# Kernel optimization log

Hardware: AMD Instinct MI355X
Metric: run time of the kernel (lower is better)

Reference implementation:

```python
import jax, jax.numpy as jnp
import numpy as np

B, L, S = 8, 8192, 512
DQ, DC = 256, 768
H, DH = 8, 64
INNER = H * DH


def setup_inputs() -> dict:
    key = jax.random.key(0)
    ks = jax.random.split(key, 8)
    std_q = 1.0 / np.sqrt(DQ)
    std_c = 1.0 / np.sqrt(DC)
    std_o = 1.0 / np.sqrt(INNER)
    return {
        "x": jax.random.normal(ks[0], (B, L, DQ), jnp.float32),
        "context": jax.random.normal(ks[1], (B, S, DC), jnp.float32),
        "seq_lens": jax.random.randint(ks[2], (B,), 1, L + 1, jnp.int32),
        "Wq": jax.random.normal(ks[3], (DQ, INNER), jnp.float32) * std_q,
        "Wk": jax.random.normal(ks[4], (DC, INNER), jnp.float32) * std_c,
        "Wv": jax.random.normal(ks[5], (DC, INNER), jnp.float32) * std_c,
        "Wo": jax.random.normal(ks[6], (INNER, DQ), jnp.float32) * std_o,
        "bo": jnp.zeros((DQ,), jnp.float32),
    }


def reference(x, context, seq_lens, Wq, Wk, Wv, Wo, bo):
    # x: [B, L, DQ] padded jagged voxel features; seq_lens: valid count per batch.
    # Equivalent to the per-batch SDPA loop: each batch's queries attend over
    # that batch's full (unmasked) context of S tokens.
    scale = 1.0 / np.sqrt(DH)
    q = (x @ Wq).reshape(B, L, H, DH).transpose(0, 2, 1, 3)        # [B,H,L,DH]
    k = (context @ Wk).reshape(B, S, H, DH).transpose(0, 2, 1, 3)  # [B,H,S,DH]
    v = (context @ Wv).reshape(B, S, H, DH).transpose(0, 2, 1, 3)  # [B,H,S,DH]
    scores = jnp.einsum("bhld,bhsd->bhls", q, k) * scale           # [B,H,L,S]
    attn = jax.nn.softmax(scores, axis=-1)
    out = jnp.einsum("bhls,bhsd->bhld", attn, v)                   # [B,H,L,DH]
    out = out.transpose(0, 2, 1, 3).reshape(B, L, INNER)
    out = out @ Wo + bo                                            # [B,L,DQ]
    valid = (jnp.arange(L)[None, :] < seq_lens[:, None])[..., None]
    return jnp.where(valid, out, 0.0)
```

## Files before the change

kernel.cpp:

```cpp
#include <hip/hip_runtime.h>
#include <hip/hip_bf16.h>

#define DEV __device__ __forceinline__

typedef float f32x4 __attribute__((ext_vector_type(4)));
typedef unsigned short u16x4 __attribute__((ext_vector_type(4)));
typedef unsigned short u16x8 __attribute__((ext_vector_type(8)));
typedef __bf16 bf16x8 __attribute__((ext_vector_type(8)));

DEV unsigned short f2b(float f) { __bf16 h = (__bf16)f; return __builtin_bit_cast(unsigned short, h); }
DEV bf16x8 asbf8(u16x8 v) { return __builtin_bit_cast(bf16x8, v); }

#define MFMA(a, b, c) __builtin_amdgcn_mfma_f32_16x16x32_bf16((a), (b), (c), 0, 0, 0)

constexpr float QSCALE = 0.18033688011112042f;
constexpr float MFIX = 20.0f;

__global__ __launch_bounds__(256) void convert_weights(
    const float* __restrict__ Wq, const float* __restrict__ Wk,
    const float* __restrict__ Wv, const float* __restrict__ Wo,
    unsigned short* __restrict__ WqT, unsigned short* __restrict__ WkvT,
    unsigned short* __restrict__ WoT)
{
  int i = blockIdx.x * 256 + threadIdx.x;
  if (i < 131072) {
    int n = i >> 8, k = i & 255;
    WqT[i] = f2b(Wq[k * 512 + n] * QSCALE);
  } else if (i < 131072 + 786432) {
    int j = i - 131072;
    int n = j / 768, k = j - n * 768;
    float v = (n < 512) ? Wk[k * 512 + n] : Wv[k * 512 + (n - 512)];
    WkvT[j] = f2b(v);
  } else {
    int j = i - 917504;
    int n = j >> 9, k = j & 511;
    WoT[j] = f2b(Wo[k * 256 + n]);
  }
}

template<int KDIM, int NCOLS, int EPI>
DEV void proj_staged(int bx, int by, unsigned short* __restrict__ Lb,
                     const float* __restrict__ Af,
                     const unsigned short* __restrict__ BT,
                     const int* __restrict__ seq_lens,
                     unsigned short* __restrict__ out0,
                     unsigned short* __restrict__ out1)
{
  constexpr int WC = NCOLS / 4;
  constexpr int NCT = WC / 16;
  constexpr int NCH = KDIM / 256;
  constexpr int RS = 264;
  const int t = threadIdx.x;
  const int wid = t >> 6, lane = t & 63;
  const int q = lane & 15, g = lane >> 4;
  const int row0 = bx * 64;
  const int wcol = by * NCOLS + wid * WC;

  if (EPI == 0) {
    const int sl = seq_lens[row0 >> 13];
    if ((row0 & 8191) >= sl) return;
  }

  const int ar0 = t >> 3, akc = (t & 7) * 4;

  const unsigned short* brow[NCT];
  #pragma unroll
  for (int ct = 0; ct < NCT; ++ct)
    brow[ct] = BT + (size_t)(wcol + ct * 16 + q) * KDIM + g * 8;

  f32x4 acc[4][NCT];
  #pragma unroll
  for (int i = 0; i < 4; ++i)
    #pragma unroll
    for (int j = 0; j < NCT; ++j) acc[i][j] = {0.f, 0.f, 0.f, 0.f};

  #pragma unroll 1
  for (int ch = 0; ch < NCH; ++ch) {
    const int kb = ch * 256;
    if (ch) __syncthreads();

    #pragma unroll
    for (int stp = 0; stp < 8; ++stp) {
      const int col = akc + 32 * stp;
      f32x4 v0 = *(const f32x4*)(Af + (size_t)(row0 + ar0) * KDIM + kb + col);
      f32x4 v1 = *(const f32x4*)(Af + (size_t)(row0 + 32 + ar0) * KDIM + kb + col);
      u16x4 w0, w1;
      w0[0] = f2b(v0[0]); w0[1] = f2b(v0[1]); w0[2] = f2b(v0[2]); w0[3] = f2b(v0[3]);
      w1[0] = f2b(v1[0]); w1[1] = f2b(v1[1]); w1[2] = f2b(v1[2]); w1[3] = f2b(v1[3]);
      *(u16x4*)(Lb + ar0 * RS + col) = w0;
      *(u16x4*)(Lb + (32 + ar0) * RS + col) = w1;
    }
    __syncthreads();

    #pragma unroll
    for (int st = 0; st < 8; ++st) {
      const int k0 = st * 32;
      bf16x8 af[4];
      #pragma unroll
      for (int rt = 0; rt < 4; ++rt)
        af[rt] = asbf8(*(const u16x8*)(Lb + (rt * 16 + q) * RS + k0 + g * 8));
      bf16x8 bf[NCT];
      #pragma unroll
      for (int ct = 0; ct < NCT; ++ct)
        bf[ct] = asbf8(*(const u16x8*)(brow[ct] + kb + k0));
      #pragma unroll
      for (int ct = 0; ct < NCT; ++ct)
        #pragma unroll
        for (int rt = 0; rt < 4; ++rt)
          acc[rt][ct] = MFMA(af[rt], bf[ct], acc[rt][ct]);
    }
  }

  if (EPI == 0) {
    const int bb = row0 >> 13, l0 = row0 & 8191;
    #pragma unroll
    for (int ct = 0; ct < NCT; ++ct) {
      int col = wcol + ct * 16 + q;
      int hh = col >> 6, d = col & 63;
      unsigned short* o = out0 + (((size_t)bb * 8 + hh) * 8192) * 64 + d;
      #pragma unroll
      for (int rt = 0; rt < 4; ++rt)
        #pragma unroll
        for (int r = 0; r < 4; ++r) {
          int ll = l0 + rt * 16 + g * 4 + r;
          o[(size_t)ll * 64] = f2b(acc[rt][ct][r]);
        }
    }
  } else {
    const int bb = row0 >> 9, s0 = row0 & 511;
    #pragma unroll
    for (int ct = 0; ct < NCT; ++ct) {
      int col = wcol + ct * 16 + q;
      if (col < 512) {
        int hh = col >> 6, d = col & 63;
        #pragma unroll
        for (int rt = 0; rt < 4; ++rt)
          #pragma unroll
          for (int r = 0; r < 4; ++r) {
            int s = s0 + rt * 16 + g * 4 + r;
            out0[(((size_t)bb * 8 + hh) * 512 + s) * 64 + d] = f2b(acc[rt][ct][r]);
          }
      } else {
        int c2 = col - 512, hh = c2 >> 6, d = c2 & 63;
        #pragma unroll
        for (int rt = 0; rt < 4; ++rt)
          #pragma unroll
          for (int r = 0; r < 4; ++r) {
            int s = s0 + rt * 16 + g * 4 + r;
            out1[(((size_t)bb * 8 + hh) * 64 + d) * 512 + s] = f2b(acc[rt][ct][r]);
          }
      }
    }
  }
}

__global__ __launch_bounds__(256, 4) void qkv_proj(
    const float* __restrict__ x, const float* __restrict__ ctx,
    const unsigned short* __restrict__ WqT, const unsigned short* __restrict__ WkvT,
    const int* __restrict__ seq_lens,
    unsigned short* __restrict__ Qws, unsigned short* __restrict__ Kws,
    unsigned short* __restrict__ VTws)
{
  __shared__ __align__(16) unsigned short Lb[64 * 264];
  const int bid = blockIdx.x;
  if (bid < 512) {
    proj_staged<768, 128, 1>(bid & 63, bid >> 6, Lb,
                             ctx, WkvT, seq_lens, Kws, VTws);
  } else {
    const int j = bid - 512;
    proj_staged<256, 128, 0>(j >> 2, j & 3, Lb,
                             x, WqT, seq_lens, Qws, nullptr);
  }
}

__global__ __launch_bounds__(256, 4) void o_proj(
    const unsigned short* __restrict__ Ab, const unsigned short* __restrict__ WoT,
    const int* __restrict__ seq_lens, float* __restrict__ outf,
    const float* __restrict__ bo)
{
  constexpr int KDIM = 512, NCOLS = 128;
  constexpr int WC = NCOLS / 4;
  constexpr int NCT = WC / 16;
  constexpr int KSTEPS = KDIM / 32;
  constexpr int ASZ = 64 * 40 * 2;
  const int t = threadIdx.x;
  const int wid = t >> 6, lane = t & 63;
  const int q = lane & 15, g = lane >> 4;
  const int row0 = blockIdx.x * 64;
  const int wcol = blockIdx.y * NCOLS + wid * WC;

  const int sl = seq_lens[row0 >> 13];
  if ((row0 & 8191) >= sl) {
    if (blockIdx.y == 0) {
      f32x4 z = {0.f, 0.f, 0.f, 0.f};
      float* o = outf + (size_t)row0 * 256;
      #pragma unroll
      for (int i = 0; i < 16; ++i)
        *(f32x4*)(o + (size_t)(i * 256 + t) * 4) = z;
    }
    return;
  }

  __shared__ __align__(16) char smem[2 * ASZ];

  const int br0 = t >> 2, bkc = (t & 3) * 8;

  f32x4 acc[4][NCT];
  #pragma unroll
  for (int i = 0; i < 4; ++i)
    #pragma unroll
    for (int j = 0; j < NCT; ++j) acc[i][j] = {0.f, 0.f, 0.f, 0.f};

  u16x8 ab;
  ab = *(const u16x8*)(Ab + (size_t)(row0 + br0) * KDIM + bkc);
  *(u16x8*)((unsigned short*)smem + br0 * 40 + bkc) = ab;
  bf16x8 bcur[NCT];
  #pragma unroll
  for (int ct = 0; ct < NCT; ++ct)
    bcur[ct] = asbf8(*(const u16x8*)(WoT + (size_t)(wcol + ct * 16 + q) * KDIM + g * 8));
  __syncthreads();

  #pragma unroll 2
  for (int st = 0; st < KSTEPS; ++st) {
    const int cur = st & 1;
    const int k1 = (st + 1) * 32;

    if (st + 1 < KSTEPS)
      ab = *(const u16x8*)(Ab + (size_t)(row0 + br0) * KDIM + k1 + bkc);
    bf16x8 bnx[NCT];
    if (st + 1 < KSTEPS) {
      #pragma unroll
      for (int ct = 0; ct < NCT; ++ct)
        bnx[ct] = asbf8(*(const u16x8*)(WoT + (size_t)(wcol + ct * 16 + q) * KDIM + k1 + g * 8));
    }

    bf16x8 af[4];
    {
      const unsigned short* Lb = (const unsigned short*)(smem + cur * ASZ);
      #pragma unroll
      for (int rt = 0; rt < 4; ++rt)
        af[rt] = asbf8(*(const u16x8*)(Lb + (rt * 16 + q) * 40 + g * 8));
    }

    #pragma unroll
    for (int ct = 0; ct < NCT; ++ct)
      #pragma unroll
      for (int rt = 0; rt < 4; ++rt)
        acc[rt][ct] = MFMA(af[rt], bcur[ct], acc[rt][ct]);

    if (st + 1 < KSTEPS) {
      *(u16x8*)((unsigned short*)(smem + (cur ^ 1) * ASZ) + br0 * 40 + bkc) = ab;
      #pragma unroll
      for (int ct = 0; ct < NCT; ++ct) bcur[ct] = bnx[ct];
    }
    __syncthreads();
  }

  const int l0 = row0 & 8191;
  #pragma unroll
  for (int ct = 0; ct < NCT; ++ct) {
    int col = wcol + ct * 16 + q;
    float bias = bo[col];
    #pragma unroll
    for (int rt = 0; rt < 4; ++rt)
      #pragma unroll
      for (int r = 0; r < 4; ++r) {
        int ll = l0 + rt * 16 + g * 4 + r;
        float v = acc[rt][ct][r] + bias;
        outf[(size_t)(row0 + rt * 16 + g * 4 + r) * 256 + col] = (ll < sl) ? v : 0.f;
      }
  }
}

__global__ __launch_bounds__(256, 4) void attn_kernel(
    const unsigned short* __restrict__ Qw, const unsigned short* __restrict__ Kw,
    const unsigned short* __restrict__ VTw, const int* __restrict__ seq_lens,
    unsigned short* __restrict__ AO)
{
  const int bid = blockIdx.x;
  const int h = bid & 7;
  const int tile = (bid >> 3) & 63;
  const int b = bid >> 9;

  const int sl = seq_lens[b];
  const int qbase0 = tile * 128;
  if (qbase0 >= sl) return;

  const int wid = threadIdx.x >> 6, lane = threadIdx.x & 63;
  const int q = lane & 15, g = lane >> 4;

  __shared__ __align__(16) unsigned short Ks[2][32 * 64];
  __shared__ __align__(16) unsigned short Vs[2][64 * 32];

  const int krow  = (wid << 3) + (lane >> 3);
  const int kslot = (lane & 7) ^ (lane >> 3);
  const int vd    = (wid << 4) + (lane >> 2);
  const int vc    = lane & 3;
  const int vswz  = (vd >> 1) & 3;
  const int vs0   = (((2 * vc) & 3) ^ vswz) * 8 + ((vc >> 1) * 4);
  const int vs1   = (((2 * vc + 1) & 3) ^ vswz) * 8 + ((vc >> 1) * 4);
  const int vrslot = (g ^ ((q >> 1) & 3)) * 8;

  const int qbase = qbase0 + wid * 32;
  const bool wactive = qbase < sl;

  const unsigned short* Qb = Qw + (((size_t)b * 8 + h) * 8192 + qbase) * 64;
  const unsigned short* Kb = Kw + ((size_t)b * 8 + h) * (512 * 64);
  const unsigned short* Vb = VTw + ((size_t)b * 8 + h) * (64 * 512);

  bf16x8 qf[2][2];
  if (wactive) {
    #pragma unroll
    for (int qt = 0; qt < 2; ++qt)
      #pragma unroll
      for (int dc = 0; dc < 2; ++dc)
        qf[qt][dc] = asbf8(*(const u16x8*)(Qb + (qt * 16 + q) * 64 + dc * 32 + g * 8));
  }

  f32x4 acc[2][4];
  float lsum[2] = {0.f, 0.f};
  #pragma unroll
  for (int qt = 0; qt < 2; ++qt)
    #pragma unroll
    for (int dt = 0; dt < 4; ++dt) acc[qt][dt] = {0.f, 0.f, 0.f, 0.f};

  {
    u16x8 kr = *(const u16x8*)(Kb + krow * 64 + (lane & 7) * 8);
    u16x8 vr = *(const u16x8*)(Vb + vd * 512 + vc * 8);
    *(u16x8*)(&Ks[0][krow * 64 + kslot * 8]) = kr;
    u16x4 vlo, vhi;
    vlo[0] = vr[0]; vlo[1] = vr[1]; vlo[2] = vr[2]; vlo[3] = vr[3];
    vhi[0] = vr[4]; vhi[1] = vr[5]; vhi[2] = vr[6]; vhi[3] = vr[7];
    *(u16x4*)(&Vs[0][vd * 32 + vs0]) = vlo;
    *(u16x4*)(&Vs[0][vd * 32 + vs1]) = vhi;
  }
  __syncthreads();

  #pragma unroll 2
  for (int st = 0; st < 16; ++st) {
    const int cur = st & 1;
    const int scn = (st + 1) * 32;

    u16x8 kn, vn;
    if (st < 15) {
      kn = *(const u16x8*)(Kb + (scn + krow) * 64 + (lane & 7) * 8);
      vn = *(const u16x8*)(Vb + vd * 512 + scn + vc * 8);
    }

    if (wactive) {
      bf16x8 kf[2][2];
      #pragma unroll
      for (int tt = 0; tt < 2; ++tt)
        #pragma unroll
        for (int dc = 0; dc < 2; ++dc)
          kf[tt][dc] = asbf8(*(const u16x8*)(
              &Ks[cur][(tt * 16 + q) * 64 + ((dc * 4 + g) ^ (q & 7)) * 8]));

      bf16x8 va[4];
      #pragma unroll
      for (int dt = 0; dt < 4; ++dt)
        va[dt] = asbf8(*(const u16x8*)(&Vs[cur][(dt * 16 + q) * 32 + vrslot]));

      #pragma unroll
      for (int qt = 0; qt < 2; ++qt) {
        f32x4 t0 = {-MFIX, -MFIX, -MFIX, -MFIX};
        f32x4 t1 = {-MFIX, -MFIX, -MFIX, -MFIX};
        t0 = MFMA(kf[0][0], qf[qt][0], t0);
        t0 = MFMA(kf[0][1], qf[qt][1], t0);
        t1 = MFMA(kf[1][0], qf[qt][0], t1);
        t1 = MFMA(kf[1][1], qf[qt][1], t1);

        float p0 = __builtin_amdgcn_exp2f(t0[0]);
        float p1 = __builtin_amdgcn_exp2f(t0[1]);
        float p2 = __builtin_amdgcn_exp2f(t0[2]);
        float p3 = __builtin_amdgcn_exp2f(t0[3]);
        float p4 = __builtin_amdgcn_exp2f(t1[0]);
        float p5 = __builtin_amdgcn_exp2f(t1[1]);
        float p6 = __builtin_amdgcn_exp2f(t1[2]);
        float p7 = __builtin_amdgcn_exp2f(t1[3]);
        lsum[qt] += ((p0 + p1) + (p2 + p3)) + ((p4 + p5) + (p6 + p7));

        u16x8 pu;
        pu[0] = f2b(p0); pu[1] = f2b(p1); pu[2] = f2b(p2); pu[3] = f2b(p3);
        pu[4] = f2b(p4); pu[5] = f2b(p5); pu[6] = f2b(p6); pu[7] = f2b(p7);
        bf16x8 pb = asbf8(pu);

        #pragma unroll
        for (int dt = 0; dt < 4; ++dt)
          acc[qt][dt] = MFMA(va[dt], pb, acc[qt][dt]);
      }
    }

    if (st < 15) {
      const int nb = cur ^ 1;
      *(u16x8*)(&Ks[nb][krow * 64 + kslot * 8]) = kn;
      u16x4 vlo, vhi;
      vlo[0] = vn[0]; vlo[1] = vn[1]; vlo[2] = vn[2]; vlo[3] = vn[3];
      vhi[0] = vn[4]; vhi[1] = vn[5]; vhi[2] = vn[6]; vhi[3] = vn[7];
      *(u16x4*)(&Vs[nb][vd * 32 + vs0]) = vlo;
      *(u16x4*)(&Vs[nb][vd * 32 + vs1]) = vhi;
    }
    __syncthreads();
  }

  if (wactive) {
    #pragma unroll
    for (int qt = 0; qt < 2; ++qt) {
      float lt = lsum[qt];
      lt += __shfl_xor(lt, 16);
      lt += __shfl_xor(lt, 32);
      float inv = __builtin_amdgcn_rcpf(lt);
      size_t ro = ((size_t)b * 8192 + qbase + qt * 16 + q) * 512 + h * 64;
      #pragma unroll
      for (int dt = 0; dt < 4; ++dt) {
        u16x4 o;
        o[0] = f2b(acc[qt][dt][0] * inv);
        o[1] = f2b(acc[qt][dt][1] * inv);
        o[2] = f2b(acc[qt][dt][2] * inv);
        o[3] = f2b(acc[qt][dt][3] * inv);
        *(u16x4*)(AO + ro + dt * 16 + g * 4) = o;
      }
    }
  }
}

extern "C" void kernel_launch(void* const* d_in, const int* in_sizes, int n_in,
                              void* d_out, int out_size, void* d_ws, size_t ws_size,
                              hipStream_t stream) {
  const float* x   = (const float*)d_in[0];
  const float* ctx = (const float*)d_in[1];
  const int*   seq = (const int*)d_in[2];
  const float* Wq  = (const float*)d_in[3];
  const float* Wk  = (const float*)d_in[4];
  const float* Wv  = (const float*)d_in[5];
  const float* Wo  = (const float*)d_in[6];
  const float* bo  = (const float*)d_in[7];
  float* Y = (float*)d_out;

  unsigned short* ws = (unsigned short*)d_ws;
  unsigned short* WqT  = ws;
  unsigned short* WkvT = WqT + 131072;
  unsigned short* WoT  = WkvT + 786432;
  unsigned short* Qws  = WoT + 131072;
  unsigned short* Kws  = Qws + 33554432;
  unsigned short* VTws = Kws + 2097152;
  unsigned short* AOws = VTws + 2097152;

  convert_weights<<<4096, 256, 0, stream>>>(Wq, Wk, Wv, Wo, WqT, WkvT, WoT);

  qkv_proj<<<4608, 256, 0, stream>>>(x, ctx, WqT, WkvT, seq, Qws, Kws, VTws);

  attn_kernel<<<4096, 256, 0, stream>>>(Qws, Kws, VTws, seq, AOws);

  o_proj<<<dim3(1024, 2), 256, 0, stream>>>(AOws, WoT, seq, Y, bo);
}
```

Measured before the change: 146.1 us.

## Fuse Q projection into attention kernel and split out KV projection

Q projection is now computed per head inside the attention kernel, reading x directly and staging Q through shared memory, so the Q workspace write and read-back are gone. K/V projection becomes its own small kernel. Attention blocks are also remapped with a rotated tile order across batches to spread the jagged work. The trade-off is that each of the 8 heads re-reads its 32 x rows from global memory and converts them to bf16, duplicating x traffic and adding per-block prologue latency.

New measurement: 171.3 us. 1.17x slower.

```diff
diff --git a/kernel.cpp b/kernel.cpp
--- a/kernel.cpp
+++ b/kernel.cpp
@@ -38,35 +38,29 @@
   }
 }
 
-template<int KDIM, int NCOLS, int EPI>
-DEV void proj_staged(int bx, int by, unsigned short* __restrict__ Lb,
-                     const float* __restrict__ Af,
-                     const unsigned short* __restrict__ BT,
-                     const int* __restrict__ seq_lens,
-                     unsigned short* __restrict__ out0,
-                     unsigned short* __restrict__ out1)
+__global__ __launch_bounds__(256, 4) void kv_proj(
+    const float* __restrict__ ctx, const unsigned short* __restrict__ WkvT,
+    unsigned short* __restrict__ Kws, unsigned short* __restrict__ VTws)
 {
+  constexpr int KDIM = 768, NCOLS = 128;
   constexpr int WC = NCOLS / 4;
   constexpr int NCT = WC / 16;
   constexpr int NCH = KDIM / 256;
   constexpr int RS = 264;
+  __shared__ __align__(16) unsigned short Lb[64 * 264];
   const int t = threadIdx.x;
   const int wid = t >> 6, lane = t & 63;
   const int q = lane & 15, g = lane >> 4;
+  const int bx = blockIdx.x & 63, by = blockIdx.x >> 6;
   const int row0 = bx * 64;
   const int wcol = by * NCOLS + wid * WC;
 
-  if (EPI == 0) {
-    const int sl = seq_lens[row0 >> 13];
-    if ((row0 & 8191) >= sl) return;
-  }
-
   const int ar0 = t >> 3, akc = (t & 7) * 4;
 
   const unsigned short* brow[NCT];
   #pragma unroll
   for (int ct = 0; ct < NCT; ++ct)
-    brow[ct] = BT + (size_t)(wcol + ct * 16 + q) * KDIM + g * 8;
+    brow[ct] = WkvT + (size_t)(wcol + ct * 16 + q) * KDIM + g * 8;
 
   f32x4 acc[4][NCT];
   #pragma unroll
@@ -78,12 +72,11 @@
   for (int ch = 0; ch < NCH; ++ch) {
     const int kb = ch * 256;
     if (ch) __syncthreads();
-
     #pragma unroll
     for (int stp = 0; stp < 8; ++stp) {
       const int col = akc + 32 * stp;
-      f32x4 v0 = *(const f32x4*)(Af + (size_t)(row0 + ar0) * KDIM + kb + col);
-      f32x4 v1 = *(const f32x4*)(Af + (size_t)(row0 + 32 + ar0) * KDIM + kb + col);
+      f32x4 v0 = *(const f32x4*)(ctx + (size_t)(row0 + ar0) * KDIM + kb + col);
+      f32x4 v1 = *(const f32x4*)(ctx + (size_t)(row0 + 32 + ar0) * KDIM + kb + col);
       u16x4 w0, w1;
       w0[0] = f2b(v0[0]); w0[1] = f2b(v0[1]); w0[2] = f2b(v0[2]); w0[3] = f2b(v0[3]);
       w1[0] = f2b(v1[0]); w1[1] = f2b(v1[1]); w1[2] = f2b(v1[2]); w1[3] = f2b(v1[3]);
@@ -111,65 +104,227 @@
     }
   }
 
-  if (EPI == 0) {
-    const int bb = row0 >> 13, l0 = row0 & 8191;
-    #pragma unroll
-    for (int ct = 0; ct < NCT; ++ct) {
-      int col = wcol + ct * 16 + q;
+  const int bb = row0 >> 9, s0 = row0 & 511;
+  #pragma unroll
+  for (int ct = 0; ct < NCT; ++ct) {
+    int col = wcol + ct * 16 + q;
+    if (col < 512) {
       int hh = col >> 6, d = col & 63;
-      unsigned short* o = out0 + (((size_t)bb * 8 + hh) * 8192) * 64 + d;
       #pragma unroll
       for (int rt = 0; rt < 4; ++rt)
         #pragma unroll
         for (int r = 0; r < 4; ++r) {
-          int ll = l0 + rt * 16 + g * 4 + r;
-          o[(size_t)ll * 64] = f2b(acc[rt][ct][r]);
+          int s = s0 + rt * 16 + g * 4 + r;
+          Kws[(((size_t)bb * 8 + hh) * 512 + s) * 64 + d] = f2b(acc[rt][ct][r]);
         }
-    }
-  } else {
-    const int bb = row0 >> 9, s0 = row0 & 511;
-    #pragma unroll
-    for (int ct = 0; ct < NCT; ++ct) {
-      int col = wcol + ct * 16 + q;
-      if (col < 512) {
-        int hh = col >> 6, d = col & 63;
-        #pragma unroll
-        for (int rt = 0; rt < 4; ++rt)
+    } else {
+      int c2 = col - 512, hh = c2 >> 6, d = c2 & 63;
+      #pragma unroll
+      for (int rt = 0; rt < 4; ++rt)
+        #pragma unroll
+        for (int r = 0; r < 4; ++r) {
+          int s = s0 + rt * 16 + g * 4 + r;
+          VTws[(((size_t)bb * 8 + hh) * 64 + d) * 512 + s] = f2b(acc[rt][ct][r]);
+        }
+    }
+  }
+}
+
+__global__ __launch_bounds__(256, 4) void attn_kernel(
+    const float* __restrict__ x, const unsigned short* __restrict__ WqT,
+    const unsigned short* __restrict__ Kw, const unsigned short* __restrict__ VTw,
+    const int* __restrict__ seq_lens, unsigned short* __restrict__ AO)
+{
+  const int bid = blockIdx.x;
+  const int c = bid & 7;
+  const int u = bid >> 3;
+  const int h = u & 7;
+  const int k2 = u >> 3;
+  const int b = k2 >> 3;
+  const int jj = k2 & 7;
+  const int tile = ((c - b) & 7) + 8 * jj;
+
+  const int sl = seq_lens[b];
+  const int qbase0 = tile * 128;
+  if (qbase0 >= sl) return;
+
+  const int wid = threadIdx.x >> 6, lane = threadIdx.x & 63;
+  const int q = lane & 15, g = lane >> 4;
+
+  __shared__ __align__(16) unsigned short smem[9216];
+  unsigned short* Ksp = smem;
+  unsigned short* Vsp = smem + 4096;
+
+  const int krow  = (wid << 3) + (lane >> 3);
+  const int kslot = (lane & 7) ^ (lane >> 3);
+  const int vd    = (wid << 4) + (lane >> 2);
+  const int vc    = lane & 3;
+  const int vswz  = (vd >> 1) & 3;
+  const int vs0   = (((2 * vc) & 3) ^ vswz) * 8 + ((vc >> 1) * 4);
+  const int vs1   = (((2 * vc + 1) & 3) ^ vswz) * 8 + ((vc >> 1) * 4);
+  const int vrslot = (g ^ ((q >> 1) & 3)) * 8;
+
+  const int qbase = qbase0 + wid * 32;
+  const bool wactive = qbase < sl;
+
+  const unsigned short* Kb = Kw + ((size_t)b * 8 + h) * (512 * 64);
+  const unsigned short* Vb = VTw + ((size_t)b * 8 + h) * (64 * 512);
+
+  bf16x8 qf[2][2];
+  {
+    unsigned short* Qt = smem + wid * (32 * 72);
+    if (wactive) {
+      f32x4 acc_q[2][4];
+      #pragma unroll
+      for (int rt = 0; rt < 2; ++rt)
+        #pragma unroll
+        for (int ct = 0; ct < 4; ++ct) acc_q[rt][ct] = {0.f, 0.f, 0.f, 0.f};
+
+      const float* xb0 = x + ((size_t)b * 8192 + qbase) * 256;
+      #pragma unroll
+      for (int ks = 0; ks < 8; ++ks) {
+        const int k0 = ks * 32;
+        bf16x8 af[2];
+        #pragma unroll
+        for (int rt = 0; rt < 2; ++rt) {
+          const float* px = xb0 + (size_t)(rt * 16 + q) * 256 + k0 + g * 8;
+          f32x4 lo = *(const f32x4*)px;
+          f32x4 hi = *(const f32x4*)(px + 4);
+          u16x8 uu;
+          uu[0] = f2b(lo[0]); uu[1] = f2b(lo[1]); uu[2] = f2b(lo[2]); uu[3] = f2b(lo[3]);
+          uu[4] = f2b(hi[0]); uu[5] = f2b(hi[1]); uu[6] = f2b(hi[2]); uu[7] = f2b(hi[3]);
+          af[rt] = asbf8(uu);
+        }
+        bf16x8 wf[4];
+        #pragma unroll
+        for (int ct = 0; ct < 4; ++ct)
+          wf[ct] = asbf8(*(const u16x8*)(WqT + (size_t)(h * 64 + ct * 16 + q) * 256 + k0 + g * 8));
+        #pragma unroll
+        for (int ct = 0; ct < 4; ++ct)
           #pragma unroll
-          for (int r = 0; r < 4; ++r) {
-            int s = s0 + rt * 16 + g * 4 + r;
-            out0[(((size_t)bb * 8 + hh) * 512 + s) * 64 + d] = f2b(acc[rt][ct][r]);
-          }
-      } else {
-        int c2 = col - 512, hh = c2 >> 6, d = c2 & 63;
-        #pragma unroll
-        for (int rt = 0; rt < 4; ++rt)
+          for (int rt = 0; rt < 2; ++rt)
+            acc_q[rt][ct] = MFMA(af[rt], wf[ct], acc_q[rt][ct]);
+      }
+      #pragma unroll
+      for (int rt = 0; rt < 2; ++rt)
+        #pragma unroll
+        for (int ct = 0; ct < 4; ++ct)
           #pragma unroll
-          for (int r = 0; r < 4; ++r) {
-            int s = s0 + rt * 16 + g * 4 + r;
-            out1[(((size_t)bb * 8 + hh) * 64 + d) * 512 + s] = f2b(acc[rt][ct][r]);
-          }
+          for (int r = 0; r < 4; ++r)
+            Qt[(rt * 16 + g * 4 + r) * 72 + ct * 16 + q] = f2b(acc_q[rt][ct][r]);
+      #pragma unroll
+      for (int qt = 0; qt < 2; ++qt)
+        #pragma unroll
+        for (int dc = 0; dc < 2; ++dc)
+          qf[qt][dc] = asbf8(*(const u16x8*)(Qt + (qt * 16 + q) * 72 + dc * 32 + g * 8));
+    }
+  }
+  __syncthreads();
+
+  f32x4 acc[2][4];
+  float lsum[2] = {0.f, 0.f};
+  #pragma unroll
+  for (int qt = 0; qt < 2; ++qt)
+    #pragma unroll
+    for (int dt = 0; dt < 4; ++dt) acc[qt][dt] = {0.f, 0.f, 0.f, 0.f};
+
+  {
+    u16x8 kr = *(const u16x8*)(Kb + krow * 64 + (lane & 7) * 8);
+    u16x8 vr = *(const u16x8*)(Vb + vd * 512 + vc * 8);
+    *(u16x8*)(&Ksp[krow * 64 + kslot * 8]) = kr;
+    u16x4 vlo, vhi;
+    vlo[0] = vr[0]; vlo[1] = vr[1]; vlo[2] = vr[2]; vlo[3] = vr[3];
+    vhi[0] = vr[4]; vhi[1] = vr[5]; vhi[2] = vr[6]; vhi[3] = vr[7];
+    *(u16x4*)(&Vsp[vd * 32 + vs0]) = vlo;
+    *(u16x4*)(&Vsp[vd * 32 + vs1]) = vhi;
+  }
+  __syncthreads();
+
+  #pragma unroll 2
+  for (int st = 0; st < 16; ++st) {
+    const int cur = st & 1;
+    const int scn = (st + 1) * 32;
+
+    u16x8 kn, vn;
+    if (st < 15) {
+      kn = *(const u16x8*)(Kb + (scn + krow) * 64 + (lane & 7) * 8);
+      vn = *(const u16x8*)(Vb + vd * 512 + scn + vc * 8);
+    }
+
+    if (wactive) {
+      bf16x8 kf[2][2];
+      #pragma unroll
+      for (int tt = 0; tt < 2; ++tt)
+        #pragma unroll
+        for (int dc = 0; dc < 2; ++dc)
+          kf[tt][dc] = asbf8(*(const u16x8*)(
+              &Ksp[cur * 2048 + (tt * 16 + q) * 64 + ((dc * 4 + g) ^ (q & 7)) * 8]));
+
+      bf16x8 va[4];
+      #pragma unroll
+      for (int dt = 0; dt < 4; ++dt)
+        va[dt] = asbf8(*(const u16x8*)(&Vsp[cur * 2048 + (dt * 16 + q) * 32 + vrslot]));
+
+      #pragma unroll
+      for (int qt = 0; qt < 2; ++qt) {
+        f32x4 t0 = {-MFIX, -MFIX, -MFIX, -MFIX};
+        f32x4 t1 = {-MFIX, -MFIX, -MFIX, -MFIX};
+        t0 = MFMA(kf[0][0], qf[qt][0], t0);
+        t0 = MFMA(kf[0][1], qf[qt][1], t0);
+        t1 = MFMA(kf[1][0], qf[qt][0], t1);
+        t1 = MFMA(kf[1][1], qf[qt][1], t1);
+
+        float p0 = __builtin_amdgcn_exp2f(t0[0]);
+        float p1 = __builtin_amdgcn_exp2f(t0[1]);
+        float p2 = __builtin_amdgcn_exp2f(t0[2]);
+        float p3 = __builtin_amdgcn_exp2f(t0[3]);
+        float p4 = __builtin_amdgcn_exp2f(t1[0]);
+        float p5 = __builtin_amdgcn_exp2f(t1[1]);
+        float p6 = __builtin_amdgcn_exp2f(t1[2]);
+        float p7 = __builtin_amdgcn_exp2f(t1[3]);
+        lsum[qt] += ((p0 + p1) + (p2 + p3)) + ((p4 + p5) + (p6 + p7));
+
+        u16x8 pu;
+        pu[0] = f2b(p0); pu[1] = f2b(p1); pu[2] = f2b(p2); pu[3] = f2b(p3);
+        pu[4] = f2b(p4); pu[5] = f2b(p5); pu[6] = f2b(p6); pu[7] = f2b(p7);
+        bf16x8 pb = asbf8(pu);
+
+        #pragma unroll
+        for (int dt = 0; dt < 4; ++dt)
+          acc[qt][dt] = MFMA(va[dt], pb, acc[qt][dt]);
       }
     }
-  }
-}
-
-__global__ __launch_bounds__(256, 4) void qkv_proj(
-    const float* __restrict__ x, const float* __restrict__ ctx,
-    const unsigned short* __restrict__ WqT, const unsigned short* __restrict__ WkvT,
-    const int* __restrict__ seq_lens,
-    unsigned short* __restrict__ Qws, unsigned short* __restrict__ Kws,
-    unsigned short* __restrict__ VTws)
-{
-  __shared__ __align__(16) unsigned short Lb[64 * 264];
-  const int bid = blockIdx.x;
-  if (bid < 512) {
-    proj_staged<768, 128, 1>(bid & 63, bid >> 6, Lb,
-                             ctx, WkvT, seq_lens, Kws, VTws);
-  } else {
-    const int j = bid - 512;
-    proj_staged<256, 128, 0>(j >> 2, j & 3, Lb,
-                             x, WqT, seq_lens, Qws, nullptr);
+
+    if (st < 15) {
+      const int nb = cur ^ 1;
+      *(u16x8*)(&Ksp[nb * 2048 + krow * 64 + kslot * 8]) = kn;
+      u16x4 vlo, vhi;
+      vlo[0] = vn[0]; vlo[1] = vn[1]; vlo[2] = vn[2]; vlo[3] = vn[3];
+      vhi[0] = vn[4]; vhi[1] = vn[5]; vhi[2] = vn[6]; vhi[3] = vn[7];
+      *(u16x4*)(&Vsp[nb * 2048 + vd * 32 + vs0]) = vlo;
+      *(u16x4*)(&Vsp[nb * 2048 + vd * 32 + vs1]) = vhi;
+    }
+    __syncthreads();
+  }
+
+  if (wactive) {
+    #pragma unroll
+    for (int qt = 0; qt < 2; ++qt) {
+      float lt = lsum[qt];
+      lt += __shfl_xor(lt, 16);
+      lt += __shfl_xor(lt, 32);
+      float inv = __builtin_amdgcn_rcpf(lt);
+      size_t ro = ((size_t)b * 8192 + qbase + qt * 16 + q) * 512 + h * 64;
+      #pragma unroll
+      for (int dt = 0; dt < 4; ++dt) {
+        u16x4 o;
+        o[0] = f2b(acc[qt][dt][0] * inv);
+        o[1] = f2b(acc[qt][dt][1] * inv);
+        o[2] = f2b(acc[qt][dt][2] * inv);
+        o[3] = f2b(acc[qt][dt][3] * inv);
+        *(u16x4*)(AO + ro + dt * 16 + g * 4) = o;
+      }
+    }
   }
 }
 
@@ -272,158 +427,6 @@
   }
 }
 
-__global__ __launch_bounds__(256, 4) void attn_kernel(
-    const unsigned short* __restrict__ Qw, const unsigned short* __restrict__ Kw,
-    const unsigned short* __restrict__ VTw, const int* __restrict__ seq_lens,
-    unsigned short* __restrict__ AO)
-{
-  const int bid = blockIdx.x;
-  const int h = bid & 7;
-  const int tile = (bid >> 3) & 63;
-  const int b = bid >> 9;
-
-  const int sl = seq_lens[b];
-  const int qbase0 = tile * 128;
-  if (qbase0 >= sl) return;
-
-  const int wid = threadIdx.x >> 6, lane = threadIdx.x & 63;
-  const int q = lane & 15, g = lane >> 4;
-
-  __shared__ __align__(16) unsigned short Ks[2][32 * 64];
-  __shared__ __align__(16) unsigned short Vs[2][64 * 32];
-
-  const int krow  = (wid << 3) + (lane >> 3);
-  const int kslot = (lane & 7) ^ (lane >> 3);
-  const int vd    = (wid << 4) + (lane >> 2);
-  const int vc    = lane & 3;
-  const int vswz  = (vd >> 1) & 3;
-  const int vs0   = (((2 * vc) & 3) ^ vswz) * 8 + ((vc >> 1) * 4);
-  const int vs1   = (((2 * vc + 1) & 3) ^ vswz) * 8 + ((vc >> 1) * 4);
-  const int vrslot = (g ^ ((q >> 1) & 3)) * 8;
-
-  const int qbase = qbase0 + wid * 32;
-  const bool wactive = qbase < sl;
-
-  const unsigned short* Qb = Qw + (((size_t)b * 8 + h) * 8192 + qbase) * 64;
-  const unsigned short* Kb = Kw + ((size_t)b * 8 + h) * (512 * 64);
-  const unsigned short* Vb = VTw + ((size_t)b * 8 + h) * (64 * 512);
-
-  bf16x8 qf[2][2];
-  if (wactive) {
-    #pragma unroll
-    for (int qt = 0; qt < 2; ++qt)
-      #pragma unroll
-      for (int dc = 0; dc < 2; ++dc)
-        qf[qt][dc] = asbf8(*(const u16x8*)(Qb + (qt * 16 + q) * 64 + dc * 32 + g * 8));
-  }
-
-  f32x4 acc[2][4];
-  float lsum[2] = {0.f, 0.f};
-  #pragma unroll
-  for (int qt = 0; qt < 2; ++qt)
-    #pragma unroll
-    for (int dt = 0; dt < 4; ++dt) acc[qt][dt] = {0.f, 0.f, 0.f, 0.f};
-
-  {
-    u16x8 kr = *(const u16x8*)(Kb + krow * 64 + (lane & 7) * 8);
-    u16x8 vr = *(const u16x8*)(Vb + vd * 512 + vc * 8);
-    *(u16x8*)(&Ks[0][krow * 64 + kslot * 8]) = kr;
-    u16x4 vlo, vhi;
-    vlo[0] = vr[0]; vlo[1] = vr[1]; vlo[2] = vr[2]; vlo[3] = vr[3];
-    vhi[0] = vr[4]; vhi[1] = vr[5]; vhi[2] = vr[6]; vhi[3] = vr[7];
-    *(u16x4*)(&Vs[0][vd * 32 + vs0]) = vlo;
-    *(u16x4*)(&Vs[0][vd * 32 + vs1]) = vhi;
-  }
-  __syncthreads();
-
-  #pragma unroll 2
-  for (int st = 0; st < 16; ++st) {
-    const int cur = st & 1;
-    const int scn = (st + 1) * 32;
-
-    u16x8 kn, vn;
-    if (st < 15) {
-      kn = *(const u16x8*)(Kb + (scn + krow) * 64 + (lane & 7) * 8);
-      vn = *(const u16x8*)(Vb + vd * 512 + scn + vc * 8);
-    }
-
-    if (wactive) {
-      bf16x8 kf[2][2];
-      #pragma unroll
-      for (int tt = 0; tt < 2; ++tt)
-        #pragma unroll
-        for (int dc = 0; dc < 2; ++dc)
-          kf[tt][dc] = asbf8(*(const u16x8*)(
-              &Ks[cur][(tt * 16 + q) * 64 + ((dc * 4 + g) ^ (q & 7)) * 8]));
-
-      bf16x8 va[4];
-      #pragma unroll
-      for (int dt = 0; dt < 4; ++dt)
-        va[dt] = asbf8(*(const u16x8*)(&Vs[cur][(dt * 16 + q) * 32 + vrslot]));
-
-      #pragma unroll
-      for (int qt = 0; qt < 2; ++qt) {
-        f32x4 t0 = {-MFIX, -MFIX, -MFIX, -MFIX};
-        f32x4 t1 = {-MFIX, -MFIX, -MFIX, -MFIX};
-        t0 = MFMA(kf[0][0], qf[qt][0], t0);
-        t0 = MFMA(kf[0][1], qf[qt][1], t0);
-        t1 = MFMA(kf[1][0], qf[qt][0], t1);
-        t1 = MFMA(kf[1][1], qf[qt][1], t1);
-
-        float p0 = __builtin_amdgcn_exp2f(t0[0]);
-        float p1 = __builtin_amdgcn_exp2f(t0[1]);
-        float p2 = __builtin_amdgcn_exp2f(t0[2]);
-        float p3 = __builtin_amdgcn_exp2f(t0[3]);
-        float p4 = __builtin_amdgcn_exp2f(t1[0]);
-        float p5 = __builtin_amdgcn_exp2f(t1[1]);
-        float p6 = __builtin_amdgcn_exp2f(t1[2]);
-        float p7 = __builtin_amdgcn_exp2f(t1[3]);
-        lsum[qt] += ((p0 + p1) + (p2 + p3)) + ((p4 + p5) + (p6 + p7));
-
-        u16x8 pu;
-        pu[0] = f2b(p0); pu[1] = f2b(p1); pu[2] = f2b(p2); pu[3] = f2b(p3);
-        pu[4] = f2b(p4); pu[5] = f2b(p5); pu[6] = f2b(p6); pu[7] = f2b(p7);
-        bf16x8 pb = asbf8(pu);
-
-        #pragma unroll
-        for (int dt = 0; dt < 4; ++dt)
-          acc[qt][dt] = MFMA(va[dt], pb, acc[qt][dt]);
-      }
-    }
-
-    if (st < 15) {
-      const int nb = cur ^ 1;
-      *(u16x8*)(&Ks[nb][krow * 64 + kslot * 8]) = kn;
-      u16x4 vlo, vhi;
-      vlo[0] = vn[0]; vlo[1] = vn[1]; vlo[2] = vn[2]; vlo[3] = vn[3];
-      vhi[0] = vn[4]; vhi[1] = vn[5]; vhi[2] = vn[6]; vhi[3] = vn[7];
-      *(u16x4*)(&Vs[nb][vd * 32 + vs0]) = vlo;
-      *(u16x4*)(&Vs[nb][vd * 32 + vs1]) = vhi;
-    }
-    __syncthreads();
-  }
-
-  if (wactive) {
-    #pragma unroll
-    for (int qt = 0; qt < 2; ++qt) {
-      float lt = lsum[qt];
-      lt += __shfl_xor(lt, 16);
-      lt += __shfl_xor(lt, 32);
-      float inv = __builtin_amdgcn_rcpf(lt);
-      size_t ro = ((size_t)b * 8192 + qbase + qt * 16 + q) * 512 + h * 64;
-      #pragma unroll
-      for (int dt = 0; dt < 4; ++dt) {
-        u16x4 o;
-        o[0] = f2b(acc[qt][dt][0] * inv);
-        o[1] = f2b(acc[qt][dt][1] * inv);
-        o[2] = f2b(acc[qt][dt][2] * inv);
-        o[3] = f2b(acc[qt][dt][3] * inv);
-        *(u16x4*)(AO + ro + dt * 16 + g * 4) = o;
-      }
-    }
-  }
-}
-
 extern "C" void kernel_launch(void* const* d_in, const int* in_sizes, int n_in,
                               void* d_out, int out_size, void* d_ws, size_t ws_size,
                               hipStream_t stream) {
@@ -441,16 +444,15 @@
   unsigned short* WqT  = ws;
   unsigned short* WkvT = WqT + 131072;
   unsigned short* WoT  = WkvT + 786432;
-  unsigned short* Qws  = WoT + 131072;
-  unsigned short* Kws  = Qws + 33554432;
+  unsigned short* Kws  = WoT + 131072;
   unsigned short* VTws = Kws + 2097152;
   unsigned short* AOws = VTws + 2097152;
 
   convert_weights<<<4096, 256, 0, stream>>>(Wq, Wk, Wv, Wo, WqT, WkvT, WoT);
 
-  qkv_proj<<<4608, 256, 0, stream>>>(x, ctx, WqT, WkvT, seq, Qws, Kws, VTws);
-
-  attn_kernel<<<4096, 256, 0, stream>>>(Qws, Kws, VTws, seq, AOws);
+  kv_proj<<<512, 256, 0, stream>>>(ctx, WkvT, Kws, VTws);
+
+  attn_kernel<<<4096, 256, 0, stream>>>(x, WqT, Kws, VTws, seq, AOws);
 
   o_proj<<<dim3(1024, 2), 256, 0, stream>>>(AOws, WoT, seq, Y, bo);
 }
```
